# Kernel tuning notes

Hardware: AMD Instinct MI355X
Metric: run time of the kernel (lower is better)

The kernel has to match this reference:

```python
import jax, jax.numpy as jnp
import numpy as np

B, T, D, H, W = 4, 2048, 256, 512, 32
EPS = 1e-5


def _xavier(key, fan_in, fan_out):
    # torch xavier_uniform on weight [out, in]; stored here as [in, out]
    limit = float(np.sqrt(6.0 / (fan_in + fan_out)))
    return jax.random.uniform(key, (fan_in, fan_out), jnp.float32, -limit, limit)


def _bias(key, fan_in, fan_out):
    # torch Linear default bias init: U(-1/sqrt(fan_in), 1/sqrt(fan_in))
    limit = float(1.0 / np.sqrt(fan_in))
    return jax.random.uniform(key, (fan_out,), jnp.float32, -limit, limit)


def setup_inputs() -> dict:
    key = jax.random.key(0)
    ks = jax.random.split(key, 16)
    inp = {
        "feature": jax.random.normal(ks[0], (B, T, D), jnp.float32),
        "gamma": jnp.ones((D,), jnp.float32),
        "beta": jnp.zeros((D,), jnp.float32),
        "w1": _xavier(ks[1], D, H), "b1": _bias(ks[2], D, H),
        "w2": _xavier(ks[3], H, H), "b2": _bias(ks[4], H, H),
        "w3": _xavier(ks[5], D, H), "b3": _bias(ks[6], H, H),
        "w4": _xavier(ks[7], H, H), "b4": _bias(ks[8], H, H),
        "w5": _xavier(ks[9], D, H), "b5": _bias(ks[10], H, H),
        "w6": _xavier(ks[11], H, H), "b6": _bias(ks[12], H, H),
        "window": W,
    }
    return inp


def reference(feature, gamma, beta, w1, b1, w2, b2, w3, b3, w4, b4, w5, b5, w6, b6, window):
    Bsz, Tlen, Din = feature.shape
    nb = Tlen // window
    x = feature.reshape(Bsz, nb, window, Din)  # [B, nb, W, D] window blocks

    # LayerNorm over last dim
    mu = jnp.mean(x, axis=-1, keepdims=True)
    var = jnp.mean((x - mu) ** 2, axis=-1, keepdims=True)
    n = (x - mu) * jax.lax.rsqrt(var + EPS) * gamma + beta

    Q = jnp.tanh(n @ w1 + b1) @ w2 + b2  # [B, nb, W, H]
    K = jnp.tanh(n @ w3 + b3) @ w4 + b4
    V = jax.nn.relu(n @ w5 + b5) @ w6 + b6

    Hdim = w2.shape[1]
    sqrt_feat = jnp.sqrt(jnp.float32(Hdim))
    sqrt_time = jnp.sqrt(jnp.float32(window))

    # time-axis attention: [B, nb, W, W]
    beta_time = jnp.einsum('bnwh,bnvh->bnwv', Q, K) / sqrt_feat
    # feature-axis attention: [B, nb, H, H]
    beta_feat = jnp.einsum('bnwh,bnwg->bnhg', Q, K) / sqrt_time

    A_time = jax.nn.softmax(beta_time, axis=-1)
    A_feat = jax.nn.softmax(beta_feat, axis=-2)

    feat = jnp.einsum('bnwh,bnhg->bnwg', V, A_feat)   # V @ A_feat
    out = jnp.einsum('bnwv,bnvg->bnwg', A_time, feat)  # A_time @ (V @ A_feat)
    return out.reshape(Bsz, Tlen, Hdim)
```

## Files before the change

### kernel.cpp

```cpp
#include <hip/hip_runtime.h>
#include <hip/hip_bf16.h>

typedef unsigned short u16;
typedef __attribute__((ext_vector_type(8))) unsigned short ushort8;
typedef __attribute__((ext_vector_type(8))) short short8;
typedef __attribute__((ext_vector_type(4))) float f32x4;
typedef __attribute__((ext_vector_type(4))) unsigned uint4_t;

#define DEV __device__ __forceinline__

DEV float b2f(u16 u){ return __uint_as_float(((unsigned)u) << 16); }
DEV u16 f2b(float f){
  unsigned x = __float_as_uint(f);
  return (u16)((x + 0x7fffu + ((x >> 16) & 1u)) >> 16);
}
DEV unsigned cvtpk(float lo, float hi){
  unsigned r;
  asm("v_cvt_pk_bf16_f32 %0, %1, %2" : "=v"(r) : "v"(lo), "v"(hi));
  return r;
}
DEV void pl32swap(unsigned& a, unsigned& b){
  asm("v_permlane32_swap_b32 %0, %1" : "+v"(a), "+v"(b));
}
DEV void pl16swap(unsigned& a, unsigned& b){
  asm("v_permlane16_swap_b32 %0, %1" : "+v"(a), "+v"(b));
}
DEV short8 ld8(const u16* p){ return __builtin_bit_cast(short8, *(const ushort8*)p); }
DEV f32x4 mfma(short8 a, short8 b, f32x4 c){
  return __builtin_amdgcn_mfma_f32_16x16x32_bf16(a, b, c, 0, 0, 0);
}
DEV float fast_tanh(float x){
  float e = __expf(2.f * x);
  return 1.f - 2.f / (e + 1.f);
}
DEV unsigned pk2(float lo, float hi){
  return (unsigned)f2b(lo) | ((unsigned)f2b(hi) << 16);
}

__global__ __launch_bounds__(256) void prep_k(
    const float* __restrict__ w1, const float* __restrict__ w2,
    const float* __restrict__ w3, const float* __restrict__ w4,
    const float* __restrict__ w5, const float* __restrict__ w6,
    u16* __restrict__ ws,
    const float* __restrict__ xg, const float* __restrict__ gg,
    const float* __restrict__ bgm, u16* __restrict__ ng)
{
  __shared__ u16 tile[64][72];
  const int bid = blockIdx.x;
  if (bid < 384) {
    const int z = bid / 64, rem = bid % 64, by = rem / 8, bx = rem % 8;
    const float* w; u16* wt; int K;
    switch (z) {
      case 0:  w = w1; wt = ws;          K = 256; break;
      case 1:  w = w2; wt = ws + 131072; K = 512; break;
      case 2:  w = w3; wt = ws + 393216; K = 256; break;
      case 3:  w = w4; wt = ws + 524288; K = 512; break;
      case 4:  w = w5; wt = ws + 786432; K = 256; break;
      default: w = w6; wt = ws + 917504; K = 512; break;
    }
    int k0 = by * 64;
    if (k0 >= K) return;
    int n0 = bx * 64;
    int t = threadIdx.x;
    int r = t >> 2, c0 = (t & 3) * 16;
    const float* src = w + (size_t)(k0 + r) * 512 + n0 + c0;
    #pragma unroll
    for (int jj = 0; jj < 4; ++jj) {
      float4 v = *(const float4*)(src + jj * 4);
      unsigned* tp = (unsigned*)&tile[r][c0 + jj*4];
      tp[0] = cvtpk(v.x, v.y);
      tp[1] = cvtpk(v.z, v.w);
    }
    __syncthreads();
    ushort8 o0, o1;
    #pragma unroll
    for (int j = 0; j < 8; ++j) { o0[j] = tile[c0 + j][r]; o1[j] = tile[c0 + 8 + j][r]; }
    u16* dst = wt + (size_t)(n0 + r) * K + k0 + c0;
    *(ushort8*)dst       = o0;
    *(ushort8*)(dst + 8) = o1;
  } else {
    const int lb = bid - 384;
    int row = lb * 8 + (threadIdx.x >> 5);
    int l32 = threadIdx.x & 31;
    const float* xr = xg + (size_t)row*256 + l32*8;
    float xf[8];
    #pragma unroll
    for (int j = 0; j < 8; j += 4) {
      float4 v = *(const float4*)(xr + j);
      xf[j] = v.x; xf[j+1] = v.y; xf[j+2] = v.z; xf[j+3] = v.w;
    }
    float s = 0.f, ss = 0.f;
    #pragma unroll
    for (int j = 0; j < 8; ++j){ s += xf[j]; ss += xf[j]*xf[j]; }
    #pragma unroll
    for (int m = 1; m < 32; m <<= 1){ s += __shfl_xor(s, m); ss += __shfl_xor(ss, m); }
    float mean = s * (1.f/256.f);
    float var  = ss * (1.f/256.f) - mean*mean;
    float rs   = rsqrtf(var + 1e-5f);
    float r8[8];
    #pragma unroll
    for (int j = 0; j < 8; j += 4) {
      float4 gv = *(const float4*)(gg  + l32*8 + j);
      float4 bv = *(const float4*)(bgm + l32*8 + j);
      r8[j]   = (xf[j]   - mean)*rs*gv.x + bv.x;
      r8[j+1] = (xf[j+1] - mean)*rs*gv.y + bv.y;
      r8[j+2] = (xf[j+2] - mean)*rs*gv.z + bv.z;
      r8[j+3] = (xf[j+3] - mean)*rs*gv.w + bv.w;
    }
    uint4_t o;
    o[0] = cvtpk(r8[0], r8[1]); o[1] = cvtpk(r8[2], r8[3]);
    o[2] = cvtpk(r8[4], r8[5]); o[3] = cvtpk(r8[6], r8[7]);
    *(uint4_t*)(ng + (size_t)row*256 + l32*8) = o;
  }
}

template<int NS, int ACT>
__global__ __launch_bounds__(512, 4) void gemm_tile(
    const u16* __restrict__ Abase, size_t a_zstride,
    const u16* __restrict__ wst, int w_off0,
    const float* __restrict__ bz0, const float* __restrict__ bz1, const float* __restrict__ bz2,
    u16* __restrict__ Cbase)
{
  constexpr int KA = NS * 32;
  __shared__ __align__(16) u16 sm[20480];
  u16* smA = sm;
  u16* smB = sm + 10240;
  const int z = blockIdx.z;
  const u16* A = Abase + (size_t)z * a_zstride;
  const u16* W = wst + w_off0 + z * 393216;
  const float* bias = (z == 0) ? bz0 : ((z == 1) ? bz1 : bz2);
  u16* C = Cbase + (size_t)z * 4194304;
  const int M0 = blockIdx.x * 128, N0 = blockIdx.y * 128;
  const int tid = threadIdx.x;
  const int wv = tid >> 6, ln = tid & 63, q = ln >> 4, r16 = ln & 15;
  const int m0w = (wv >> 2) * 64, n0w = (wv & 3) * 32;
  const f32x4 Z = {0.f, 0.f, 0.f, 0.f};

  const int srow = tid >> 2, scq = (tid & 3) * 8;
  const u16* gA = A + (size_t)(M0 + srow) * KA + scq;
  const u16* gB = W + (size_t)(N0 + srow) * KA + scq;
  u16* dA = smA + srow * 40 + scq;
  u16* dB = smB + srow * 40 + scq;

  ushort8 rA[2], rB[2];
  rA[0] = *(const ushort8*)gA;
  rB[0] = *(const ushort8*)gB;
  *(ushort8*)dA = rA[0];
  *(ushort8*)dB = rB[0];
  if (NS > 1) { rA[1] = *(const ushort8*)(gA + 32); rB[1] = *(const ushort8*)(gB + 32); }
  __syncthreads();

  f32x4 acc[4][2];
  #pragma unroll
  for (int mf = 0; mf < 4; ++mf){ acc[mf][0] = Z; acc[mf][1] = Z; }

  #pragma unroll
  for (int kk = 0; kk < NS; ++kk) {
    const int cur = kk & 1;
    const u16* bufA = smA + cur * 5120;
    const u16* bufB = smB + cur * 5120;
    short8 aF[4], bF[2];
    #pragma unroll
    for (int mf = 0; mf < 4; ++mf) aF[mf] = ld8(bufA + (m0w + mf*16 + r16)*40 + q*8);
    #pragma unroll
    for (int nf = 0; nf < 2; ++nf) bF[nf] = ld8(bufB + (n0w + nf*16 + r16)*40 + q*8);
    #pragma unroll
    for (int mf = 0; mf < 4; ++mf)
      #pragma unroll
      for (int nf = 0; nf < 2; ++nf)
        acc[mf][nf] = mfma(aF[mf], bF[nf], acc[mf][nf]);
    if (kk + 1 < NS) {
      *(ushort8*)(dA + (cur ^ 1) * 5120) = rA[(kk + 1) & 1];
      *(ushort8*)(dB + (cur ^ 1) * 5120) = rB[(kk + 1) & 1];
    }
    if (kk + 2 < NS) {
      rA[kk & 1] = *(const ushort8*)(gA + (kk + 2) * 32);
      rB[kk & 1] = *(const ushort8*)(gB + (kk + 2) * 32);
    }
    __syncthreads();
  }

  u16* ct = sm;
  #pragma unroll
  for (int nf = 0; nf < 2; ++nf) {
    int colL = n0w + nf*16 + r16;
    float bs = bias[N0 + colL];
    #pragma unroll
    for (int mf = 0; mf < 4; ++mf)
      #pragma unroll
      for (int i = 0; i < 4; ++i) {
        int row = m0w + mf*16 + q*4 + i;
        float v = acc[mf][nf][i] + bs;
        if (ACT == 1) v = fmaxf(v, 0.f);
        else if (ACT == 3) v = (z == 2) ? fmaxf(v, 0.f) : fast_tanh(v);
        ct[row*132 + colL] = f2b(v);
      }
  }
  __syncthreads();
  #pragma unroll
  for (int j = 0; j < 4; ++j) {
    int row = (tid >> 4) + j*32;
    int cb2 = (tid & 15) * 8;
    ushort8 vv = *(const ushort8*)(ct + row*132 + cb2);
    *(ushort8*)(C + (size_t)(M0 + row)*512 + N0 + cb2) = vv;
  }
}

#define AV   0
#define AQT  16640
#define AKT  37120
#define ABT  57600
#define AAT  59712
#define ASM_ELS 60992

__global__ __launch_bounds__(1024) void attn_k(
    const u16* __restrict__ QKVg, float* __restrict__ outg)
{
  __shared__ __align__(16) u16 sm[ASM_ELS];
  const int tid = threadIdx.x;
  const int bid = blockIdx.x;
  const int wv = tid >> 6, ln = tid & 63, q = ln >> 4, r16 = ln & 15;
  const f32x4 Z = {0.f, 0.f, 0.f, 0.f};
  const float RS512 = 0.04419417382415922f;
  const float C32L2 = 0.25500526676986233f;
  const u16* Qg = QKVg + (size_t)bid * 16384;
  const u16* Kg = QKVg + 4194304 + (size_t)bid * 16384;
  const u16* Vg = QKVg + 8388608 + (size_t)bid * 16384;

  float* btf = (float*)(sm + ABT);
  if (wv < 4) {
    int mt = wv >> 1, nt = wv & 1;
    f32x4 acc = Z;
    const u16* qb = Qg + (mt*16 + r16)*512;
    const u16* kb = Kg + (nt*16 + r16)*512;
    #pragma unroll
    for (int kk = 0; kk < 16; ++kk)
      acc = mfma(ld8(qb + kk*32 + q*8), ld8(kb + kk*32 + q*8), acc);
    #pragma unroll
    for (int i = 0; i < 4; ++i)
      btf[(mt*16 + q*4 + i)*33 + nt*16 + r16] = acc[i] * RS512;
  } else if (wv < 12) {
    int t1 = tid - 256;
    int rp = t1 & 15;
    int cb = (t1 >> 4) * 16;
    const u16* s0 = Qg + (2*rp)*512 + cb;
    const u16* s1 = s0 + 512;
    ushort8 a0 = *(const ushort8*)s0, a1 = *(const ushort8*)(s0 + 8);
    ushort8 c0v = *(const ushort8*)s1, c1v = *(const ushort8*)(s1 + 8);
    unsigned* qt32 = (unsigned*)(sm + AQT);
    #pragma unroll
    for (int j = 0; j < 8; ++j) {
      qt32[(cb + j)*20 + rp]     = (unsigned)a0[j] | ((unsigned)c0v[j] << 16);
      qt32[(cb + 8 + j)*20 + rp] = (unsigned)a1[j] | ((unsigned)c1v[j] << 16);
    }
  } else {
    int t2 = tid - 768;
    int vrow = t2 >> 3, seg = (t2 & 7) * 64;
    const u16* src = Vg + vrow*512 + seg;
    #pragma unroll
    for (int jj = 0; jj < 8; ++jj)
      *(ushort8*)(sm + AV + vrow*520 + seg + jj*8) = *(const ushort8*)(src + jj*8);
  }
  __syncthreads();

  if (tid < 512) {
    int row = tid >> 4, v2 = tid & 15;
    float v0 = btf[row*33 + v2], v1 = btf[row*33 + v2 + 16];
    float m = fmaxf(v0, v1);
    #pragma unroll
    for (int msk = 1; msk < 16; msk <<= 1) m = fmaxf(m, __shfl_xor(m, msk));
    float e0 = __expf(v0 - m), e1 = __expf(v1 - m);
    float sum = e0 + e1;
    #pragma unroll
    for (int msk = 1; msk < 16; msk <<= 1) sum += __shfl_xor(sum, msk);
    float inv = 1.f / sum;
    sm[AAT + row*40 + v2]      = f2b(e0 * inv);
    sm[AAT + row*40 + v2 + 16] = f2b(e1 * inv);
  } else {
    int t1 = tid - 512;
    int rp = t1 & 15;
    int cb = (t1 >> 4) * 16;
    const u16* s0 = Kg + (2*rp)*512 + cb;
    const u16* s1 = s0 + 512;
    ushort8 a0 = *(const ushort8*)s0, a1 = *(const ushort8*)(s0 + 8);
    ushort8 c0v = *(const ushort8*)s1, c1v = *(const ushort8*)(s1 + 8);
    unsigned* kt32 = (unsigned*)(sm + AKT);
    #pragma unroll
    for (int j = 0; j < 8; ++j) {
      kt32[(cb + j)*20 + rp]     = (unsigned)a0[j] | ((unsigned)c0v[j] << 16);
      kt32[(cb + 8 + j)*20 + rp] = (unsigned)a1[j] | ((unsigned)c1v[j] << 16);
    }
  }
  __syncthreads();

  {
    const int g0 = wv * 32;
    f32x4 facc[2][2];
    facc[0][0]=Z; facc[0][1]=Z; facc[1][0]=Z; facc[1][1]=Z;
    float csum[2] = {0.f, 0.f};
    short8 bK[2];
    #pragma unroll
    for (int gt = 0; gt < 2; ++gt)
      bK[gt] = ld8(sm + AKT + (size_t)(g0 + gt*16 + r16)*40 + q*8);

    #pragma unroll 2
    for (int ht = 0; ht < 16; ++ht) {
      f32x4 sv[2][2];
      #pragma unroll
      for (int smi = 0; smi < 2; ++smi) {
        short8 aQ = ld8(sm + AQT + (ht*32 + smi*16 + r16)*40 + q*8);
        #pragma unroll
        for (int gt = 0; gt < 2; ++gt)
          sv[smi][gt] = mfma(aQ, bK[gt], Z);
      }
      unsigned D[2][4];
      #pragma unroll
      for (int gt = 0; gt < 2; ++gt) {
        float e[2][4];
        #pragma unroll
        for (int smi = 0; smi < 2; ++smi)
          #pragma unroll
          for (int i = 0; i < 4; ++i) {
            float ev = exp2f(sv[smi][gt][i] * C32L2);
            e[smi][i] = ev;
            csum[gt] += ev;
          }
        #pragma unroll
        for (int k = 0; k < 2; ++k) {
          unsigned w0 = cvtpk(e[0][2*k], e[0][2*k+1]);
          unsigned w1 = cvtpk(e[1][2*k], e[1][2*k+1]);
          pl32swap(w0, w1);
          pl16swap(w0, w1);
          D[gt][k]     = w0;
          D[gt][k + 2] = w1;
        }
      }
      #pragma unroll
      for (int mt = 0; mt < 2; ++mt) {
        short8 aV = ld8(sm + AV + (mt*16 + r16)*520 + ht*32 + q*8);
        #pragma unroll
        for (int gt = 0; gt < 2; ++gt) {
          uint4_t dv = {D[gt][0], D[gt][1], D[gt][2], D[gt][3]};
          short8 bE = __builtin_bit_cast(short8, dv);
          facc[mt][gt] = mfma(aV, bE, facc[mt][gt]);
        }
      }
    }
    float inv[2];
    #pragma unroll
    for (int gt = 0; gt < 2; ++gt) {
      float cs = csum[gt];
      cs += __shfl_xor(cs, 16);
      cs += __shfl_xor(cs, 32);
      inv[gt] = 1.f / cs;
    }
    unsigned F[2][4];
    #pragma unroll
    for (int gt = 0; gt < 2; ++gt) {
      float e0n[4], e1n[4];
      #pragma unroll
      for (int i = 0; i < 4; ++i) {
        e0n[i] = facc[0][gt][i] * inv[gt];
        e1n[i] = facc[1][gt][i] * inv[gt];
      }
      #pragma unroll
      for (int k = 0; k < 2; ++k) {
        unsigned w0 = cvtpk(e0n[2*k], e0n[2*k+1]);
        unsigned w1 = cvtpk(e1n[2*k], e1n[2*k+1]);
        pl32swap(w0, w1);
        pl16swap(w0, w1);
        F[gt][k]     = w0;
        F[gt][k + 2] = w1;
      }
    }
    short8 aA0 = ld8(sm + AAT + r16*40 + q*8);
    short8 aA1 = ld8(sm + AAT + (16 + r16)*40 + q*8);
    #pragma unroll
    for (int gt = 0; gt < 2; ++gt) {
      uint4_t fv = {F[gt][0], F[gt][1], F[gt][2], F[gt][3]};
      short8 bF = __builtin_bit_cast(short8, fv);
      f32x4 o0 = mfma(aA0, bF, Z);
      f32x4 o1 = mfma(aA1, bF, Z);
      #pragma unroll
      for (int i = 0; i < 4; ++i) {
        int g = g0 + gt*16 + r16;
        outg[(size_t)(bid*32 + q*4 + i)*512 + g]      = o0[i];
        outg[(size_t)(bid*32 + 16 + q*4 + i)*512 + g] = o1[i];
      }
    }
  }
}


#define OFF_V   0
#define OFF_N   16640
#define OFF_T   25088
#define OFF_Q   41728
#define OFF_K   58368
#define OFF_BT  75008
#define OFF_QT  16640
#define OFF_KT  37120
#define OFF_AT  78080
#define OFF_FT  37120
#define SMEM_ELS 79360

template<int ACT>
DEV void mlp_branch(const u16* __restrict__ nl, u16* __restrict__ tl, u16* __restrict__ ol,
                    const u16* __restrict__ wA, const float* __restrict__ bA,
                    const u16* __restrict__ wB, const float* __restrict__ bB,
                    int wv, int q, int r16)
{
  const f32x4 Z = {0.f, 0.f, 0.f, 0.f};
  const int c0 = wv*32 + r16;
  float biasA0 = bA[c0], biasA1 = bA[c0 + 16];
  float biasB0 = bB[c0], biasB1 = bB[c0 + 16];
  {
    const u16* cp0 = wA + (size_t)c0*256 + q*8;
    const u16* cp1 = cp0 + 16*256;
    const u16* a0p = nl + r16 * 264 + q*8;
    const u16* a1p = nl + (16 + r16) * 264 + q*8;
    f32x4 acc[2][2];
    acc[0][0]=Z; acc[0][1]=Z; acc[1][0]=Z; acc[1][1]=Z;
    #pragma unroll
    for (int kk = 0; kk < 8; ++kk) {
      short8 a0 = ld8(a0p + kk*32);
      short8 a1 = ld8(a1p + kk*32);
      short8 b0 = ld8(cp0 + kk*32);
      short8 b1 = ld8(cp1 + kk*32);
      acc[0][0] = mfma(a0, b0, acc[0][0]);
      acc[1][0] = mfma(a1, b0, acc[1][0]);
      acc[0][1] = mfma(a0, b1, acc[0][1]);
      acc[1][1] = mfma(a1, b1, acc[1][1]);
    }
    #pragma unroll
    for (int gt = 0; gt < 2; ++gt) {
      float bias = gt ? biasA1 : biasA0;
      #pragma unroll
      for (int mt = 0; mt < 2; ++mt)
        #pragma unroll
        for (int i = 0; i < 4; ++i) {
          float v = acc[mt][gt][i] + bias;
          v = (ACT == 0) ? fast_tanh(v) : fmaxf(v, 0.f);
          tl[(mt*16 + q*4 + i)*520 + c0 + gt*16] = f2b(v);
        }
    }
  }
  __syncthreads();
  {
    const u16* cp0 = wB + (size_t)c0*512 + q*8;
    const u16* cp1 = cp0 + 16*512;
    const u16* a0p = tl + r16 * 520 + q*8;
    const u16* a1p = tl + (16 + r16) * 520 + q*8;
    f32x4 acc[2][2];
    acc[0][0]=Z; acc[0][1]=Z; acc[1][0]=Z; acc[1][1]=Z;
    #pragma unroll
    for (int kk = 0; kk < 16; ++kk) {
      short8 a0 = ld8(a0p + kk*32);
      short8 a1 = ld8(a1p + kk*32);
      short8 b0 = ld8(cp0 + kk*32);
      short8 b1 = ld8(cp1 + kk*32);
      acc[0][0] = mfma(a0, b0, acc[0][0]);
      acc[1][0] = mfma(a1, b0, acc[1][0]);
      acc[0][1] = mfma(a0, b1, acc[0][1]);
      acc[1][1] = mfma(a1, b1, acc[1][1]);
    }
    #pragma unroll
    for (int gt = 0; gt < 2; ++gt) {
      float bias = gt ? biasB1 : biasB0;
      #pragma unroll
      for (int mt = 0; mt < 2; ++mt)
        #pragma unroll
        for (int i = 0; i < 4; ++i)
          ol[(mt*16 + q*4 + i)*520 + c0 + gt*16] = f2b(acc[mt][gt][i] + bias);
    }
  }
}

__global__ __launch_bounds__(1024) void fused_main(
    const float* __restrict__ xg, const float* __restrict__ gg, const float* __restrict__ bgm,
    const float* __restrict__ b1, const float* __restrict__ b2, const float* __restrict__ b3,
    const float* __restrict__ b4, const float* __restrict__ b5, const float* __restrict__ b6,
    const u16* __restrict__ wst, float* __restrict__ outg)
{
  __shared__ __align__(16) u16 sm[SMEM_ELS];
  const int tid = threadIdx.x;
  const int bid = blockIdx.x;
  const int wv = tid >> 6, ln = tid & 63, q = ln >> 4, r16 = ln & 15;
  const f32x4 Z = {0.f, 0.f, 0.f, 0.f};
  const float RS512 = 0.04419417382415922f;
  const float C32L2 = 0.25500526676986233f;

  {
    int row = tid >> 5, l32 = tid & 31;
    const float* xr = xg + (size_t)(bid*32 + row)*256 + l32*8;
    float xf[8];
    #pragma unroll
    for (int j = 0; j < 8; j += 4) {
      float4 v = *(const float4*)(xr + j);
      xf[j] = v.x; xf[j+1] = v.y; xf[j+2] = v.z; xf[j+3] = v.w;
    }
    float s = 0.f, ss = 0.f;
    #pragma unroll
    for (int j = 0; j < 8; ++j){ s += xf[j]; ss += xf[j]*xf[j]; }
    #pragma unroll
    for (int m = 1; m < 32; m <<= 1){ s += __shfl_xor(s, m); ss += __shfl_xor(ss, m); }
    float mean = s * (1.f/256.f);
    float var  = ss * (1.f/256.f) - mean*mean;
    float rs   = rsqrtf(var + 1e-5f);
    float gf[8], bf[8];
    #pragma unroll
    for (int j = 0; j < 8; j += 4) {
      float4 gv = *(const float4*)(gg  + l32*8 + j);
      float4 bv = *(const float4*)(bgm + l32*8 + j);
      gf[j] = gv.x; gf[j+1] = gv.y; gf[j+2] = gv.z; gf[j+3] = gv.w;
      bf[j] = bv.x; bf[j+1] = bv.y; bf[j+2] = bv.z; bf[j+3] = bv.w;
    }
    ushort8 o0;
    #pragma unroll
    for (int j = 0; j < 8; ++j)
      o0[j] = f2b((xf[j] - mean)*rs*gf[j] + bf[j]);
    *(ushort8*)(sm + OFF_N + row*264 + l32*8) = o0;
  }
  __syncthreads();

  mlp_branch<0>(sm+OFF_N, sm+OFF_T, sm+OFF_Q, wst,          b1, wst + 131072, b2, wv, q, r16);
  __syncthreads();
  mlp_branch<0>(sm+OFF_N, sm+OFF_T, sm+OFF_K, wst + 393216, b3, wst + 524288, b4, wv, q, r16);
  __syncthreads();
  mlp_branch<1>(sm+OFF_N, sm+OFF_T, sm+OFF_V, wst + 786432, b5, wst + 917504, b6, wv, q, r16);
  __syncthreads();

  float* btf = (float*)(sm + OFF_BT);
  if (wv < 4) {
    int mt = wv >> 1, nt = wv & 1;
    f32x4 acc = Z;
    const u16* qb = sm + OFF_Q + (mt*16 + r16)*520;
    const u16* kb = sm + OFF_K + (nt*16 + r16)*520;
    for (int kk = 0; kk < 16; ++kk)
      acc = mfma(ld8(qb + kk*32 + q*8), ld8(kb + kk*32 + q*8), acc);
    #pragma unroll
    for (int i = 0; i < 4; ++i)
      btf[(mt*16 + q*4 + i)*33 + nt*16 + r16] = acc[i] * RS512;
  } else if (wv < 12) {
    int t1 = tid - 256;
    int row = t1 & 31, cb = (t1 >> 5) * 32;
    const u16* src = sm + OFF_Q + row*520 + cb;
    ushort8 v[4];
    #pragma unroll
    for (int jj = 0; jj < 4; ++jj) v[jj] = *(const ushort8*)(src + jj*8);
    #pragma unroll
    for (int jj = 0; jj < 4; ++jj)
      #pragma unroll
      for (int j = 0; j < 8; ++j)
        sm[OFF_QT + (cb + jj*8 + j)*40 + row] = v[jj][j];
  }
  __syncthreads();

  if (tid < 512) {
    int row = tid >> 4, v2 = tid & 15;
    float v0 = btf[row*33 + v2], v1 = btf[row*33 + v2 + 16];
    float m = fmaxf(v0, v1);
    #pragma unroll
    for (int msk = 1; msk < 16; msk <<= 1) m = fmaxf(m, __shfl_xor(m, msk));
    float e0 = __expf(v0 - m), e1 = __expf(v1 - m);
    float sum = e0 + e1;
    #pragma unroll
    for (int msk = 1; msk < 16; msk <<= 1) sum += __shfl_xor(sum, msk);
    float inv = 1.f / sum;
    sm[OFF_AT + row*40 + v2]      = f2b(e0 * inv);
    sm[OFF_AT + row*40 + v2 + 16] = f2b(e1 * inv);
  } else {
    int t2 = tid - 512;
    int row = t2 & 31, cb = (t2 >> 5) * 32;
    const u16* src = sm + OFF_K + row*520 + cb;
    ushort8 v[4];
    #pragma unroll
    for (int jj = 0; jj < 4; ++jj) v[jj] = *(const ushort8*)(src + jj*8);
    #pragma unroll
    for (int jj = 0; jj < 4; ++jj)
      #pragma unroll
      for (int j = 0; j < 8; ++j)
        sm[OFF_KT + (cb + jj*8 + j)*40 + row] = v[jj][j];
  }
  __syncthreads();

  {
    const int g0 = wv * 32;
    const bool hi32 = (ln >= 32);
    const bool qodd = (q & 1);
    f32x4 facc[2][2];
    facc[0][0]=Z; facc[0][1]=Z; facc[1][0]=Z; facc[1][1]=Z;
    float csum[2] = {0.f, 0.f};
    short8 bK[2];
    #pragma unroll
    for (int gt = 0; gt < 2; ++gt)
      bK[gt] = ld8(sm + OFF_KT + (size_t)(g0 + gt*16 + r16)*40 + q*8);

    #pragma unroll 2
    for (int ht = 0; ht < 16; ++ht) {
      f32x4 sv[2][2];
      #pragma unroll
      for (int smi = 0; smi < 2; ++smi) {
        short8 aQ = ld8(sm + OFF_QT + (ht*32 + smi*16 + r16)*40 + q*8);
        #pragma unroll
        for (int gt = 0; gt < 2; ++gt)
          sv[smi][gt] = mfma(aQ, bK[gt], Z);
      }
      unsigned D[2][4];
      #pragma unroll
      for (int gt = 0; gt < 2; ++gt) {
        float e[2][4];
        #pragma unroll
        for (int smi = 0; smi < 2; ++smi)
          #pragma unroll
          for (int i = 0; i < 4; ++i) {
            float ev = exp2f(sv[smi][gt][i] * C32L2);
            e[smi][i] = ev;
            csum[gt] += ev;
          }
        #pragma unroll
        for (int k = 0; k < 2; ++k) {
          unsigned w0 = pk2(e[0][2*k], e[0][2*k+1]);
          unsigned w1 = pk2(e[1][2*k], e[1][2*k+1]);
          unsigned Pw0 = (unsigned)__shfl_xor((int)w0, 32);
          unsigned Pw1 = (unsigned)__shfl_xor((int)w1, 32);
          unsigned x = hi32 ? Pw1 : w0;
          unsigned y = hi32 ? w1 : Pw0;
          unsigned xs = (unsigned)__shfl_xor((int)x, 16);
          unsigned ys = (unsigned)__shfl_xor((int)y, 16);
          D[gt][k]     = qodd ? ys : x;
          D[gt][k + 2] = qodd ? y  : xs;
        }
      }
      #pragma unroll
      for (int mt = 0; mt < 2; ++mt) {
        short8 aV = ld8(sm + OFF_V + (mt*16 + r16)*520 + ht*32 + q*8);
        #pragma unroll
        for (int gt = 0; gt < 2; ++gt) {
          uint4_t dv = {D[gt][0], D[gt][1], D[gt][2], D[gt][3]};
          short8 bE = __builtin_bit_cast(short8, dv);
          facc[mt][gt] = mfma(aV, bE, facc[mt][gt]);
        }
      }
    }
    float inv[2];
    #pragma unroll
    for (int gt = 0; gt < 2; ++gt) {
      float cs = csum[gt];
      cs += __shfl_xor(cs, 16);
      cs += __shfl_xor(cs, 32);
      inv[gt] = 1.f / cs;
    }
    #pragma unroll
    for (int mt = 0; mt < 2; ++mt)
      #pragma unroll
      for (int gt = 0; gt < 2; ++gt)
        #pragma unroll
        for (int i = 0; i < 4; ++i) {
          int w = mt*16 + q*4 + i;
          int g = g0 + gt*16 + r16;
          sm[OFF_FT + g*40 + w] = f2b(facc[mt][gt][i] * inv[gt]);
        }
  }

  {
    const int g0 = wv * 32;
    short8 aA0 = ld8(sm + OFF_AT + r16*40 + q*8);
    short8 aA1 = ld8(sm + OFF_AT + (16 + r16)*40 + q*8);
    #pragma unroll
    for (int gt = 0; gt < 2; ++gt) {
      short8 bF = ld8(sm + OFF_FT + (size_t)(g0 + gt*16 + r16)*40 + q*8);
      f32x4 o0 = mfma(aA0, bF, Z);
      f32x4 o1 = mfma(aA1, bF, Z);
      #pragma unroll
      for (int i = 0; i < 4; ++i) {
        int g = g0 + gt*16 + r16;
        outg[(size_t)(bid*32 + q*4 + i)*512 + g]      = o0[i];
        outg[(size_t)(bid*32 + 16 + q*4 + i)*512 + g] = o1[i];
      }
    }
  }
}


extern "C" void kernel_launch(void* const* d_in, const int* in_sizes, int n_in,
                              void* d_out, int out_size, void* d_ws, size_t ws_size,
                              hipStream_t stream)
{
  const float* x  = (const float*)d_in[0];
  const float* gm = (const float*)d_in[1];
  const float* bt = (const float*)d_in[2];
  const float* w1 = (const float*)d_in[3];
  const float* b1 = (const float*)d_in[4];
  const float* w2 = (const float*)d_in[5];
  const float* b2 = (const float*)d_in[6];
  const float* w3 = (const float*)d_in[7];
  const float* b3 = (const float*)d_in[8];
  const float* w4 = (const float*)d_in[9];
  const float* b4 = (const float*)d_in[10];
  const float* w5 = (const float*)d_in[11];
  const float* b5 = (const float*)d_in[12];
  const float* w6 = (const float*)d_in[13];
  const float* b6 = (const float*)d_in[14];
  u16* ws  = (u16*)d_ws;
  float* out = (float*)d_out;

  const size_t WT_OFF  = 0;
  const size_t N_OFF   = 1179648;
  const size_t T_OFF   = 3276800;
  const size_t QKV_OFF = 15859712;
  const size_t NEED_BYTES = 28442624ULL * 2ULL;

  if (ws_size >= NEED_BYTES) {
    prep_k<<<1408, 256, 0, stream>>>(w1, w2, w3, w4, w5, w6, ws + WT_OFF,
                                     x, gm, bt, ws + N_OFF);
    gemm_tile<8, 3><<<dim3(64, 4, 3), 512, 0, stream>>>(
        ws + N_OFF, 0, ws + WT_OFF, 0, b1, b3, b5, ws + T_OFF);
    gemm_tile<16, 2><<<dim3(64, 4, 3), 512, 0, stream>>>(
        ws + T_OFF, 4194304, ws + WT_OFF, 131072, b2, b4, b6, ws + QKV_OFF);
    attn_k<<<256, 1024, 0, stream>>>(ws + QKV_OFF, out);
  } else {
    prep_k<<<384, 256, 0, stream>>>(w1, w2, w3, w4, w5, w6, ws + WT_OFF,
                                    x, gm, bt, ws + WT_OFF );
    fused_main<<<256, 1024, 0, stream>>>(x, gm, bt, b1, b2, b3, b4, b5, b6, ws + WT_OFF, out);
  }
}
```

Baseline: 80.17 us.

## Split attention kernel across two feature halves per window with smaller blocks

The attention kernel now runs two 512-thread blocks per window, each computing half of the output feature columns, instead of one 1024-thread block per window. V is no longer staged in shared memory but read directly from global memory inside the loop, and the transposed Q/K tiles use a tighter padding stride, so shared memory per block is roughly halved and more blocks can be resident. The costs are that both blocks redundantly recompute the time-attention softmax and transpose all of Q, and that the V reads now go through global/L2 in the hot loop.

```diff
diff --git a/kernel.cpp b/kernel.cpp
--- a/kernel.cpp
+++ b/kernel.cpp
@@ -3,6 +3,7 @@
 
 typedef unsigned short u16;
 typedef __attribute__((ext_vector_type(8))) unsigned short ushort8;
+typedef __attribute__((ext_vector_type(4))) unsigned short ushort4_t;
 typedef __attribute__((ext_vector_type(8))) short short8;
 typedef __attribute__((ext_vector_type(4))) float f32x4;
 typedef __attribute__((ext_vector_type(4))) unsigned uint4_t;
@@ -26,6 +27,14 @@
   asm("v_permlane16_swap_b32 %0, %1" : "+v"(a), "+v"(b));
 }
 DEV short8 ld8(const u16* p){ return __builtin_bit_cast(short8, *(const ushort8*)p); }
+DEV short8 ld8s(const u16* p){
+  ushort4_t a = *(const ushort4_t*)p;
+  ushort4_t b = *(const ushort4_t*)(p + 4);
+  ushort8 v;
+  #pragma unroll
+  for (int j = 0; j < 4; ++j){ v[j] = a[j]; v[j+4] = b[j]; }
+  return __builtin_bit_cast(short8, v);
+}
 DEV f32x4 mfma(short8 a, short8 b, f32x4 c){
   return __builtin_amdgcn_mfma_f32_16x16x32_bf16(a, b, c, 0, 0, 0);
 }
@@ -206,28 +215,28 @@
   }
 }
 
-#define AV   0
-#define AQT  16640
-#define AKT  37120
-#define ABT  57600
-#define AAT  59712
-#define ASM_ELS 60992
-
-__global__ __launch_bounds__(1024) void attn_k(
+#define AQT2  0
+#define AKT2  18432
+#define ABT2  27648
+#define AAT2  29760
+#define ASM2_ELS 31040
+
+__global__ __launch_bounds__(512, 4) void attn_k2(
     const u16* __restrict__ QKVg, float* __restrict__ outg)
 {
-  __shared__ __align__(16) u16 sm[ASM_ELS];
+  __shared__ __align__(16) u16 sm[ASM2_ELS];
   const int tid = threadIdx.x;
   const int bid = blockIdx.x;
+  const int win = bid >> 1, hb = bid & 1;
   const int wv = tid >> 6, ln = tid & 63, q = ln >> 4, r16 = ln & 15;
   const f32x4 Z = {0.f, 0.f, 0.f, 0.f};
   const float RS512 = 0.04419417382415922f;
   const float C32L2 = 0.25500526676986233f;
-  const u16* Qg = QKVg + (size_t)bid * 16384;
-  const u16* Kg = QKVg + 4194304 + (size_t)bid * 16384;
-  const u16* Vg = QKVg + 8388608 + (size_t)bid * 16384;
-
-  float* btf = (float*)(sm + ABT);
+  const u16* Qg = QKVg + (size_t)win * 16384;
+  const u16* Kg = QKVg + 4194304 + (size_t)win * 16384;
+  const u16* Vg = QKVg + 8388608 + (size_t)win * 16384;
+
+  float* btf = (float*)(sm + ABT2);
   if (wv < 4) {
     int mt = wv >> 1, nt = wv & 1;
     f32x4 acc = Z;
@@ -239,56 +248,56 @@
     #pragma unroll
     for (int i = 0; i < 4; ++i)
       btf[(mt*16 + q*4 + i)*33 + nt*16 + r16] = acc[i] * RS512;
-  } else if (wv < 12) {
+  } else {
+    int t1 = tid - 256;
+    int rp = t1 & 15;
+    unsigned* qt32 = (unsigned*)(sm + AQT2);
+    #pragma unroll
+    for (int h2 = 0; h2 < 2; ++h2) {
+      int cb = (t1 >> 4) * 16 + h2 * 256;
+      const u16* s0 = Qg + (2*rp)*512 + cb;
+      const u16* s1 = s0 + 512;
+      ushort8 a0 = *(const ushort8*)s0, a1 = *(const ushort8*)(s0 + 8);
+      ushort8 c0v = *(const ushort8*)s1, c1v = *(const ushort8*)(s1 + 8);
+      #pragma unroll
+      for (int j = 0; j < 8; ++j) {
+        qt32[(cb + j)*18 + rp]     = (unsigned)a0[j] | ((unsigned)c0v[j] << 16);
+        qt32[(cb + 8 + j)*18 + rp] = (unsigned)a1[j] | ((unsigned)c1v[j] << 16);
+      }
+    }
+  }
+  __syncthreads();
+
+  if (tid < 256) {
+    int row = tid >> 3, t8 = tid & 7;
+    int c = t8 * 4;
+    float v0 = btf[row*33 + c + 0], v1 = btf[row*33 + c + 1];
+    float v2 = btf[row*33 + c + 2], v3 = btf[row*33 + c + 3];
+    float m = fmaxf(fmaxf(v0, v1), fmaxf(v2, v3));
+    #pragma unroll
+    for (int msk = 1; msk < 8; msk <<= 1) m = fmaxf(m, __shfl_xor(m, msk));
+    float e0 = __expf(v0 - m), e1 = __expf(v1 - m);
+    float e2 = __expf(v2 - m), e3 = __expf(v3 - m);
+    float sum = (e0 + e1) + (e2 + e3);
+    #pragma unroll
+    for (int msk = 1; msk < 8; msk <<= 1) sum += __shfl_xor(sum, msk);
+    float inv = 1.f / sum;
+    unsigned* at32 = (unsigned*)(sm + AAT2);
+    at32[(row*40 + c)/2]     = cvtpk(e0 * inv, e1 * inv);
+    at32[(row*40 + c)/2 + 1] = cvtpk(e2 * inv, e3 * inv);
+  } else {
     int t1 = tid - 256;
     int rp = t1 & 15;
     int cb = (t1 >> 4) * 16;
-    const u16* s0 = Qg + (2*rp)*512 + cb;
+    const u16* s0 = Kg + (2*rp)*512 + hb*256 + cb;
     const u16* s1 = s0 + 512;
     ushort8 a0 = *(const ushort8*)s0, a1 = *(const ushort8*)(s0 + 8);
     ushort8 c0v = *(const ushort8*)s1, c1v = *(const ushort8*)(s1 + 8);
-    unsigned* qt32 = (unsigned*)(sm + AQT);
+    unsigned* kt32 = (unsigned*)(sm + AKT2);
     #pragma unroll
     for (int j = 0; j < 8; ++j) {
-      qt32[(cb + j)*20 + rp]     = (unsigned)a0[j] | ((unsigned)c0v[j] << 16);
-      qt32[(cb + 8 + j)*20 + rp] = (unsigned)a1[j] | ((unsigned)c1v[j] << 16);
-    }
-  } else {
-    int t2 = tid - 768;
-    int vrow = t2 >> 3, seg = (t2 & 7) * 64;
-    const u16* src = Vg + vrow*512 + seg;
-    #pragma unroll
-    for (int jj = 0; jj < 8; ++jj)
-      *(ushort8*)(sm + AV + vrow*520 + seg + jj*8) = *(const ushort8*)(src + jj*8);
-  }
-  __syncthreads();
-
-  if (tid < 512) {
-    int row = tid >> 4, v2 = tid & 15;
-    float v0 = btf[row*33 + v2], v1 = btf[row*33 + v2 + 16];
-    float m = fmaxf(v0, v1);
-    #pragma unroll
-    for (int msk = 1; msk < 16; msk <<= 1) m = fmaxf(m, __shfl_xor(m, msk));
-    float e0 = __expf(v0 - m), e1 = __expf(v1 - m);
-    float sum = e0 + e1;
-    #pragma unroll
-    for (int msk = 1; msk < 16; msk <<= 1) sum += __shfl_xor(sum, msk);
-    float inv = 1.f / sum;
-    sm[AAT + row*40 + v2]      = f2b(e0 * inv);
-    sm[AAT + row*40 + v2 + 16] = f2b(e1 * inv);
-  } else {
-    int t1 = tid - 512;
-    int rp = t1 & 15;
-    int cb = (t1 >> 4) * 16;
-    const u16* s0 = Kg + (2*rp)*512 + cb;
-    const u16* s1 = s0 + 512;
-    ushort8 a0 = *(const ushort8*)s0, a1 = *(const ushort8*)(s0 + 8);
-    ushort8 c0v = *(const ushort8*)s1, c1v = *(const ushort8*)(s1 + 8);
-    unsigned* kt32 = (unsigned*)(sm + AKT);
-    #pragma unroll
-    for (int j = 0; j < 8; ++j) {
-      kt32[(cb + j)*20 + rp]     = (unsigned)a0[j] | ((unsigned)c0v[j] << 16);
-      kt32[(cb + 8 + j)*20 + rp] = (unsigned)a1[j] | ((unsigned)c1v[j] << 16);
+      kt32[(cb + j)*18 + rp]     = (unsigned)a0[j] | ((unsigned)c0v[j] << 16);
+      kt32[(cb + 8 + j)*18 + rp] = (unsigned)a1[j] | ((unsigned)c1v[j] << 16);
     }
   }
   __syncthreads();
@@ -301,14 +310,18 @@
     short8 bK[2];
     #pragma unroll
     for (int gt = 0; gt < 2; ++gt)
-      bK[gt] = ld8(sm + AKT + (size_t)(g0 + gt*16 + r16)*40 + q*8);
+      bK[gt] = ld8s(sm + AKT2 + (g0 + gt*16 + r16)*36 + q*8);
 
     #pragma unroll 2
     for (int ht = 0; ht < 16; ++ht) {
+      short8 aV[2];
+      #pragma unroll
+      for (int mt = 0; mt < 2; ++mt)
+        aV[mt] = ld8(Vg + (mt*16 + r16)*512 + ht*32 + q*8);
       f32x4 sv[2][2];
       #pragma unroll
       for (int smi = 0; smi < 2; ++smi) {
-        short8 aQ = ld8(sm + AQT + (ht*32 + smi*16 + r16)*40 + q*8);
+        short8 aQ = ld8s(sm + AQT2 + (ht*32 + smi*16 + r16)*36 + q*8);
         #pragma unroll
         for (int gt = 0; gt < 2; ++gt)
           sv[smi][gt] = mfma(aQ, bK[gt], Z);
@@ -336,15 +349,13 @@
         }
       }
       #pragma unroll
-      for (int mt = 0; mt < 2; ++mt) {
-        short8 aV = ld8(sm + AV + (mt*16 + r16)*520 + ht*32 + q*8);
+      for (int mt = 0; mt < 2; ++mt)
         #pragma unroll
         for (int gt = 0; gt < 2; ++gt) {
           uint4_t dv = {D[gt][0], D[gt][1], D[gt][2], D[gt][3]};
           short8 bE = __builtin_bit_cast(short8, dv);
-          facc[mt][gt] = mfma(aV, bE, facc[mt][gt]);
+          facc[mt][gt] = mfma(aV[mt], bE, facc[mt][gt]);
         }
-      }
     }
     float inv[2];
     #pragma unroll
@@ -373,8 +384,8 @@
         F[gt][k + 2] = w1;
       }
     }
-    short8 aA0 = ld8(sm + AAT + r16*40 + q*8);
-    short8 aA1 = ld8(sm + AAT + (16 + r16)*40 + q*8);
+    short8 aA0 = ld8(sm + AAT2 + r16*40 + q*8);
+    short8 aA1 = ld8(sm + AAT2 + (16 + r16)*40 + q*8);
     #pragma unroll
     for (int gt = 0; gt < 2; ++gt) {
       uint4_t fv = {F[gt][0], F[gt][1], F[gt][2], F[gt][3]};
@@ -383,9 +394,9 @@
       f32x4 o1 = mfma(aA1, bF, Z);
       #pragma unroll
       for (int i = 0; i < 4; ++i) {
-        int g = g0 + gt*16 + r16;
-        outg[(size_t)(bid*32 + q*4 + i)*512 + g]      = o0[i];
-        outg[(size_t)(bid*32 + 16 + q*4 + i)*512 + g] = o1[i];
+        int gg = hb*256 + g0 + gt*16 + r16;
+        outg[(size_t)(win*32 + q*4 + i)*512 + gg]      = o0[i];
+        outg[(size_t)(win*32 + 16 + q*4 + i)*512 + gg] = o1[i];
       }
     }
   }
@@ -718,7 +729,7 @@
         ws + N_OFF, 0, ws + WT_OFF, 0, b1, b3, b5, ws + T_OFF);
     gemm_tile<16, 2><<<dim3(64, 4, 3), 512, 0, stream>>>(
         ws + T_OFF, 4194304, ws + WT_OFF, 131072, b2, b4, b6, ws + QKV_OFF);
-    attn_k<<<256, 1024, 0, stream>>>(ws + QKV_OFF, out);
+    attn_k2<<<512, 512, 0, stream>>>(ws + QKV_OFF, out);
   } else {
     prep_k<<<384, 256, 0, stream>>>(w1, w2, w3, w4, w5, w6, ws + WT_OFF,
                                     x, gm, bt, ws + WT_OFF );
```

Result: slower. 83.66 us (+4.4%).
